# Performance work log

Hardware: AMD Instinct MI355X
Metric: run time of the kernel (lower is better)

The kernel has to match this reference:

```python
import jax, jax.numpy as jnp
import numpy as np
import math


def setup_inputs() -> dict:
    key = jax.random.key(0)
    k1, k2, k3 = jax.random.split(key, 3)
    b, h, w = 4, 64, 64
    hw = h * w
    gp_dim = 64
    sim_matrix = jax.random.normal(k1, (b, hw, hw), dtype=jnp.float32)
    conv_w = jax.random.normal(k2, (gp_dim, 2), dtype=jnp.float32)
    conv_b = jax.random.normal(k3, (gp_dim,), dtype=jnp.float32)
    return {"sim_matrix": sim_matrix, "conv_w": conv_w, "conv_b": conv_b,
            "b": b, "h": h, "w": w}


def _pos_enc(conv_w, conv_b, b, h, w):
    # normalized grid coords in (-1, 1), channel 0 = x (width), channel 1 = y (height)
    ys = jnp.linspace(-1.0 + 1.0 / h, 1.0 - 1.0 / h, h, dtype=jnp.float32)
    xs = jnp.linspace(-1.0 + 1.0 / w, 1.0 - 1.0 / w, w, dtype=jnp.float32)
    gy, gx = jnp.meshgrid(ys, xs, indexing="ij")          # [h, w] each
    coords = jnp.stack([gx, gy], axis=0)                   # [2, h, w]
    # 1x1 conv == per-pixel linear: [d,2] @ [2,h,w] + bias
    proj = jnp.einsum("dc,chw->dhw", conv_w, coords) + conv_b[:, None, None]
    f = jnp.cos(8.0 * math.pi * proj)                       # fourier basis, [d, h, w]
    return jnp.broadcast_to(f[None], (b,) + f.shape)        # [b, d, h, w]


def reference(sim_matrix, conv_w, conv_b, b, h, w):
    d = conv_w.shape[0]
    f = _pos_enc(conv_w, conv_b, b, h, w)                   # [b, d, h, w]
    f = f.reshape(b, d, h * w).transpose(0, 2, 1)           # [b, hw, d]
    conf = jax.nn.softmax(sim_matrix, axis=2)               # [b, hw, hw]
    gp = jnp.einsum("bnm,bmd->bnd", conf, f)                # [b, hw, d]
    return gp.transpose(0, 2, 1).reshape(b, d, h, w)        # [b, d, h, w]
```

## Files before the change

### kernel.cpp

```cpp
#include <hip/hip_runtime.h>


typedef _Float16 f16;
typedef f16 f16x8 __attribute__((ext_vector_type(8)));
typedef float f32x4 __attribute__((ext_vector_type(4)));

static constexpr int HW = 4096;
static constexpr int ND = 64;
static constexpr int KW = 8;
static constexpr int KM = HW / KW;

__global__ __launch_bounds__(256) void posenc_f16(
    const float* __restrict__ cw, const float* __restrict__ cb,
    f16* __restrict__ ft)
{
    int g = blockIdx.x * 256 + threadIdx.x;
    int d = g >> 12;
    int m = g & 4095;
    int i = m >> 6;
    int j = m & 63;
    float gx = (float)(2 * j - 63) * (1.0f / 64.0f);
    float gy = (float)(2 * i - 63) * (1.0f / 64.0f);
    float proj = cw[2 * d] * gx + cw[2 * d + 1] * gy + cb[d];
    float v = cosf(25.132741228718345f * proj);
    ft[(size_t)d * HW + m] = (f16)v;
}

__global__ __launch_bounds__(512) void gp_main(
    const float* __restrict__ sim, const f16* __restrict__ ft,
    float* __restrict__ out)
{
    const int bb   = blockIdx.x >> 8;
    const int nt   = blockIdx.x & 255;
    const int wv   = threadIdx.x >> 6;
    const int lane = threadIdx.x & 63;
    const int c    = lane & 15;
    const int q    = lane >> 4;
    const int n0   = nt * 16;

    const float* srow  = sim + (size_t)bb * HW * HW + (size_t)(n0 + c) * HW
                             + wv * KM + q * 8;
    const f16*   fbase = ft + (size_t)c * HW + wv * KM + q * 8;

    f32x4 acc0 = {0.f, 0.f, 0.f, 0.f};
    f32x4 acc1 = {0.f, 0.f, 0.f, 0.f};
    f32x4 acc2 = {0.f, 0.f, 0.f, 0.f};
    f32x4 acc3 = {0.f, 0.f, 0.f, 0.f};
    float psum = 0.0f;

    #pragma unroll 4
    for (int m0 = 0; m0 < KM; m0 += 32) {
        f32x4 s0 = *(const f32x4*)(srow + m0);
        f32x4 s1 = *(const f32x4*)(srow + m0 + 4);

        float p0 = __expf(s0[0]);
        float p1 = __expf(s0[1]);
        float p2 = __expf(s0[2]);
        float p3 = __expf(s0[3]);
        float p4 = __expf(s1[0]);
        float p5 = __expf(s1[1]);
        float p6 = __expf(s1[2]);
        float p7 = __expf(s1[3]);
        psum += ((p0 + p1) + (p2 + p3)) + ((p4 + p5) + (p6 + p7));

        f16x8 a;
        a[0] = (f16)p0; a[1] = (f16)p1; a[2] = (f16)p2; a[3] = (f16)p3;
        a[4] = (f16)p4; a[5] = (f16)p5; a[6] = (f16)p6; a[7] = (f16)p7;

        f16x8 b0 = *(const f16x8*)(fbase + (size_t)(0 * 16) * HW + m0);
        f16x8 b1 = *(const f16x8*)(fbase + (size_t)(1 * 16) * HW + m0);
        f16x8 b2 = *(const f16x8*)(fbase + (size_t)(2 * 16) * HW + m0);
        f16x8 b3 = *(const f16x8*)(fbase + (size_t)(3 * 16) * HW + m0);

        acc0 = __builtin_amdgcn_mfma_f32_16x16x32_f16(a, b0, acc0, 0, 0, 0);
        acc1 = __builtin_amdgcn_mfma_f32_16x16x32_f16(a, b1, acc1, 0, 0, 0);
        acc2 = __builtin_amdgcn_mfma_f32_16x16x32_f16(a, b2, acc2, 0, 0, 0);
        acc3 = __builtin_amdgcn_mfma_f32_16x16x32_f16(a, b3, acc3, 0, 0, 0);
    }

    __shared__ f32x4 red[4][KW][64];
    __shared__ float redsum[KW][64];
    red[0][wv][lane] = acc0;
    red[1][wv][lane] = acc1;
    red[2][wv][lane] = acc2;
    red[3][wv][lane] = acc3;
    redsum[wv][lane] = psum;
    __syncthreads();

    if (wv < 2) {
        const int t0 = wv * 2, t1 = wv * 2 + 1;
        f32x4 A0 = {0.f, 0.f, 0.f, 0.f};
        f32x4 A1 = {0.f, 0.f, 0.f, 0.f};
        float ps = 0.0f;
        #pragma unroll
        for (int s = 0; s < KW; s++) {
            A0 += red[t0][s][lane];
            A1 += red[t1][s][lane];
            ps += redsum[s][lane];
        }
        ps += __shfl_xor(ps, 16, 64);
        ps += __shfl_xor(ps, 32, 64);
        float r0 = 1.0f / __shfl(ps, q * 4 + 0, 64);
        float r1 = 1.0f / __shfl(ps, q * 4 + 1, 64);
        float r2 = 1.0f / __shfl(ps, q * 4 + 2, 64);
        float r3 = 1.0f / __shfl(ps, q * 4 + 3, 64);

        float* ob = out + (size_t)bb * ND * HW + (size_t)c * HW + n0 + q * 4;
        {
            f32x4 v; v[0] = A0[0] * r0; v[1] = A0[1] * r1;
                     v[2] = A0[2] * r2; v[3] = A0[3] * r3;
            *(f32x4*)(ob + (size_t)t0 * 16 * HW) = v;
        }
        {
            f32x4 v; v[0] = A1[0] * r0; v[1] = A1[1] * r1;
                     v[2] = A1[2] * r2; v[3] = A1[3] * r3;
            *(f32x4*)(ob + (size_t)t1 * 16 * HW) = v;
        }
    }
}

extern "C" void kernel_launch(void* const* d_in, const int* in_sizes, int n_in,
                              void* d_out, int out_size, void* d_ws, size_t ws_size,
                              hipStream_t stream) {
    (void)in_sizes; (void)n_in; (void)out_size; (void)ws_size;
    const float* sim = (const float*)d_in[0];
    const float* cw  = (const float*)d_in[1];
    const float* cb  = (const float*)d_in[2];
    float* out = (float*)d_out;
    f16* ft = (f16*)d_ws;

    posenc_f16<<<(ND * HW) / 256, 256, 0, stream>>>(cw, cb, ft);
    gp_main<<<1024, 512, 0, stream>>>(sim, ft, out);
}
```

Measured before the change: 384.1 us.

## Process four row tiles per block to reuse positional-encoding fragments

Each block now covers 64 rows instead of 16 and keeps a 4x4 grid of MFMA accumulators. Each f16 positional-encoding fragment loaded per K step is reused across four row tiles, which cuts B-operand loads fourfold. The cross-wave reduction runs in two phases through shared memory, and the grid shrinks from 1024 to 256 blocks. In exchange, fewer waves are resident to hide the latency of the large fp32 sim stream, register pressure rises, and the outer loop is no longer unrolled.

New measurement: 371.0 us. 1.04x faster.

```diff
diff --git a/kernel.cpp b/kernel.cpp
--- a/kernel.cpp
+++ b/kernel.cpp
@@ -30,74 +30,88 @@
     const float* __restrict__ sim, const f16* __restrict__ ft,
     float* __restrict__ out)
 {
-    const int bb   = blockIdx.x >> 8;
-    const int nt   = blockIdx.x & 255;
+    const int bb   = blockIdx.x >> 6;
+    const int ng   = blockIdx.x & 63;
     const int wv   = threadIdx.x >> 6;
     const int lane = threadIdx.x & 63;
     const int c    = lane & 15;
     const int q    = lane >> 4;
-    const int n0   = nt * 16;
+    const int n0   = ng * 64;
 
-    const float* srow  = sim + (size_t)bb * HW * HW + (size_t)(n0 + c) * HW
+    const float* sbase = sim + (size_t)bb * HW * HW + (size_t)(n0 + c) * HW
                              + wv * KM + q * 8;
     const f16*   fbase = ft + (size_t)c * HW + wv * KM + q * 8;
 
-    f32x4 acc0 = {0.f, 0.f, 0.f, 0.f};
-    f32x4 acc1 = {0.f, 0.f, 0.f, 0.f};
-    f32x4 acc2 = {0.f, 0.f, 0.f, 0.f};
-    f32x4 acc3 = {0.f, 0.f, 0.f, 0.f};
-    float psum = 0.0f;
+    f32x4 acc[4][4];
+    #pragma unroll
+    for (int t = 0; t < 4; t++)
+        #pragma unroll
+        for (int u = 0; u < 4; u++)
+            acc[t][u] = (f32x4){0.f, 0.f, 0.f, 0.f};
+    float psum[4] = {0.f, 0.f, 0.f, 0.f};
 
-    #pragma unroll 4
     for (int m0 = 0; m0 < KM; m0 += 32) {
-        f32x4 s0 = *(const f32x4*)(srow + m0);
-        f32x4 s1 = *(const f32x4*)(srow + m0 + 4);
+        f16x8 bfr[4];
+        #pragma unroll
+        for (int u = 0; u < 4; u++)
+            bfr[u] = *(const f16x8*)(fbase + (size_t)u * 16 * HW + m0);
 
-        float p0 = __expf(s0[0]);
-        float p1 = __expf(s0[1]);
-        float p2 = __expf(s0[2]);
-        float p3 = __expf(s0[3]);
-        float p4 = __expf(s1[0]);
-        float p5 = __expf(s1[1]);
-        float p6 = __expf(s1[2]);
-        float p7 = __expf(s1[3]);
-        psum += ((p0 + p1) + (p2 + p3)) + ((p4 + p5) + (p6 + p7));
+        #pragma unroll
+        for (int t = 0; t < 4; t++) {
+            const float* sp = sbase + (size_t)t * 16 * HW + m0;
+            f32x4 s0 = *(const f32x4*)sp;
+            f32x4 s1 = *(const f32x4*)(sp + 4);
 
-        f16x8 a;
-        a[0] = (f16)p0; a[1] = (f16)p1; a[2] = (f16)p2; a[3] = (f16)p3;
-        a[4] = (f16)p4; a[5] = (f16)p5; a[6] = (f16)p6; a[7] = (f16)p7;
+            float p0 = __expf(s0[0]);
+            float p1 = __expf(s0[1]);
+            float p2 = __expf(s0[2]);
+            float p3 = __expf(s0[3]);
+            float p4 = __expf(s1[0]);
+            float p5 = __expf(s1[1]);
+            float p6 = __expf(s1[2]);
+            float p7 = __expf(s1[3]);
+            psum[t] += ((p0 + p1) + (p2 + p3)) + ((p4 + p5) + (p6 + p7));
 
-        f16x8 b0 = *(const f16x8*)(fbase + (size_t)(0 * 16) * HW + m0);
-        f16x8 b1 = *(const f16x8*)(fbase + (size_t)(1 * 16) * HW + m0);
-        f16x8 b2 = *(const f16x8*)(fbase + (size_t)(2 * 16) * HW + m0);
-        f16x8 b3 = *(const f16x8*)(fbase + (size_t)(3 * 16) * HW + m0);
+            f16x8 a;
+            a[0] = (f16)p0; a[1] = (f16)p1; a[2] = (f16)p2; a[3] = (f16)p3;
+            a[4] = (f16)p4; a[5] = (f16)p5; a[6] = (f16)p6; a[7] = (f16)p7;
 
-        acc0 = __builtin_amdgcn_mfma_f32_16x16x32_f16(a, b0, acc0, 0, 0, 0);
-        acc1 = __builtin_amdgcn_mfma_f32_16x16x32_f16(a, b1, acc1, 0, 0, 0);
-        acc2 = __builtin_amdgcn_mfma_f32_16x16x32_f16(a, b2, acc2, 0, 0, 0);
-        acc3 = __builtin_amdgcn_mfma_f32_16x16x32_f16(a, b3, acc3, 0, 0, 0);
+            #pragma unroll
+            for (int u = 0; u < 4; u++)
+                acc[t][u] = __builtin_amdgcn_mfma_f32_16x16x32_f16(
+                    a, bfr[u], acc[t][u], 0, 0, 0);
+        }
     }
 
-    __shared__ f32x4 red[4][KW][64];
-    __shared__ float redsum[KW][64];
-    red[0][wv][lane] = acc0;
-    red[1][wv][lane] = acc1;
-    red[2][wv][lane] = acc2;
-    red[3][wv][lane] = acc3;
-    redsum[wv][lane] = psum;
-    __syncthreads();
+    __shared__ f32x4 red[KW][8][64];
+    __shared__ float rsum[KW][4][64];
 
-    if (wv < 2) {
-        const int t0 = wv * 2, t1 = wv * 2 + 1;
-        f32x4 A0 = {0.f, 0.f, 0.f, 0.f};
-        f32x4 A1 = {0.f, 0.f, 0.f, 0.f};
-        float ps = 0.0f;
+    #pragma unroll
+    for (int t = 0; t < 4; t++)
+        rsum[wv][t][lane] = psum[t];
+
+    #pragma unroll
+    for (int ph = 0; ph < 2; ph++) {
+        const int tb = ph * 2;
+        if (ph)
+            __syncthreads();
         #pragma unroll
-        for (int s = 0; s < KW; s++) {
-            A0 += red[t0][s][lane];
-            A1 += red[t1][s][lane];
-            ps += redsum[s][lane];
-        }
+        for (int t = 0; t < 2; t++)
+            #pragma unroll
+            for (int u = 0; u < 4; u++)
+                red[wv][t * 4 + u][lane] = acc[tb + t][u];
+        __syncthreads();
+
+        const int t = tb + (wv >> 2);
+        const int u = wv & 3;
+        f32x4 A = red[0][wv][lane];
+        #pragma unroll
+        for (int s = 1; s < KW; s++)
+            A += red[s][wv][lane];
+        float ps = 0.f;
+        #pragma unroll
+        for (int s = 0; s < KW; s++)
+            ps += rsum[s][t][lane];
         ps += __shfl_xor(ps, 16, 64);
         ps += __shfl_xor(ps, 32, 64);
         float r0 = 1.0f / __shfl(ps, q * 4 + 0, 64);
@@ -105,17 +119,10 @@
         float r2 = 1.0f / __shfl(ps, q * 4 + 2, 64);
         float r3 = 1.0f / __shfl(ps, q * 4 + 3, 64);
 
-        float* ob = out + (size_t)bb * ND * HW + (size_t)c * HW + n0 + q * 4;
-        {
-            f32x4 v; v[0] = A0[0] * r0; v[1] = A0[1] * r1;
-                     v[2] = A0[2] * r2; v[3] = A0[3] * r3;
-            *(f32x4*)(ob + (size_t)t0 * 16 * HW) = v;
-        }
-        {
-            f32x4 v; v[0] = A1[0] * r0; v[1] = A1[1] * r1;
-                     v[2] = A1[2] * r2; v[3] = A1[3] * r3;
-            *(f32x4*)(ob + (size_t)t1 * 16 * HW) = v;
-        }
+        f32x4 v;
+        v[0] = A[0] * r0; v[1] = A[1] * r1; v[2] = A[2] * r2; v[3] = A[3] * r3;
+        *(f32x4*)(out + (size_t)bb * ND * HW + (size_t)(u * 16 + c) * HW
+                  + n0 + t * 16 + q * 4) = v;
     }
 }
 
@@ -130,5 +137,5 @@
     f16* ft = (f16*)d_ws;
 
     posenc_f16<<<(ND * HW) / 256, 256, 0, stream>>>(cw, cb, ft);
-    gp_main<<<1024, 512, 0, stream>>>(sim, ft, out);
+    gp_main<<<256, 512, 0, stream>>>(sim, ft, out);
 }
```
